# Kernel tuning notes

Measured on AMD Instinct MI355X. Metric: run time of the kernel, lower is better.

Reference implementation:

```python
import jax, jax.numpy as jnp
import numpy as np

B, D, P, C = 4096, 512, 256, 8
LAMBDA = 1.0


def setup_inputs() -> dict:
    key = jax.random.key(0)
    k1, k2, k3, k4 = jax.random.split(key, 4)
    x = jax.random.normal(k1, (B, D), dtype=jnp.float32)
    y = jax.random.randint(k2, (B,), 0, C, dtype=jnp.int32)
    prototypes = jax.random.normal(k3, (P, D), dtype=jnp.float32)
    # omega initialized as eye + 0.01*randn per class, like the torch module
    omega = jnp.eye(D, dtype=jnp.float32)[None] + 0.01 * jax.random.normal(k4, (C, D, D), dtype=jnp.float32)
    prototype_labels = (jnp.arange(P, dtype=jnp.int32) % C).astype(jnp.int32)
    return {"x": x, "y": y, "prototypes": prototypes, "omega": omega, "prototype_labels": prototype_labels}


def reference(x, y, prototypes, omega, prototype_labels):
    # transformed inputs per class: tx[c,b,:] = omega[c] @ x[b]
    tx = jnp.einsum('cij,bj->cbi', omega, x)                     # [C,B,D]
    # transformed prototypes under every class omega, then pick each
    # prototype's own class matrix: tp[p,:] = omega[label[p]] @ w[p]
    tp_all = jnp.einsum('cij,pj->cpi', omega, prototypes)        # [C,P,D]
    tp = tp_all[prototype_labels, jnp.arange(P)]                 # [P,D]
    # squared distances via expansion ||a-b||^2 = |a|^2 + |b|^2 - 2ab
    dots = jnp.einsum('cbd,pd->cbp', tx, tp)                     # [C,B,P]
    x2 = jnp.sum(tx * tx, axis=-1)                               # [C,B]
    p2 = jnp.sum(tp * tp, axis=-1)                               # [P]
    dist_all = x2[:, :, None] + p2[None, None, :] - 2.0 * dots   # [C,B,P]
    # each prototype uses the omega of its own class
    dist = dist_all[prototype_labels, :, jnp.arange(P)].T        # [B,P]
    same = prototype_labels[None, :] == y[:, None]               # [B,P]
    inf = jnp.float32(jnp.inf)
    pos = jnp.min(jnp.where(same, dist, inf), axis=1)            # [B]
    neg = jnp.min(jnp.where(same, inf, dist), axis=1)            # [B]
    mu = (pos - neg) / (pos + neg)
    loss = jnp.mean(jax.nn.sigmoid(LAMBDA * mu))
    loss = loss + 0.01 * jnp.linalg.norm(omega.reshape(-1))
    return loss
```

## Files before the change

### kernel.cpp

```cpp
#include <hip/hip_runtime.h>
#include <math.h>

typedef unsigned short ushort_t;
typedef __attribute__((ext_vector_type(8))) short short8;
typedef __attribute__((ext_vector_type(4))) float f32x4;

#define B_N 4096
#define D_N 512
#define P_N 256
#define C_N 8

#define ACC_OFF   0
#define P2G_OFF   256
#define X2_OFF    1280
#define XB_OFF    132352
#define OMB_OFF   (XB_OFF + B_N*D_N*2)
#define TPG_OFF   (OMB_OFF + C_N*D_N*D_N*2)
#define UG_OFF    (TPG_OFF + P_N*D_N*2)
#define OMBT_OFF  (UG_OFF + P_N*D_N*2)
#define MINB_OFF  OMBT_OFF

#define MFMA16(a, b, c) __builtin_amdgcn_mfma_f32_16x16x32_bf16(a, b, c, 0, 0, 0)

__device__ inline ushort_t f2bf(float f) {
    union { float f; unsigned u; } v; v.f = f;
    unsigned r = v.u + 0x7FFFu + ((v.u >> 16) & 1u);
    return (ushort_t)(r >> 16);
}

__device__ __forceinline__ void gll16(const ushort_t* g, ushort_t* l) {
    __builtin_amdgcn_global_load_lds((const __attribute__((address_space(1))) void*)g,
                                     (__attribute__((address_space(3))) void*)l, 16, 0, 0);
}

__global__ void k_cast_x(const float* __restrict__ x, ushort_t* __restrict__ xb) {
    int idx = blockIdx.x * 256 + threadIdx.x;
    const float4* x4 = (const float4*)x;
    float4 a = x4[idx * 2], b = x4[idx * 2 + 1];
    union { ushort_t s[8]; uint4 v; } o;
    o.s[0] = f2bf(a.x); o.s[1] = f2bf(a.y); o.s[2] = f2bf(a.z); o.s[3] = f2bf(a.w);
    o.s[4] = f2bf(b.x); o.s[5] = f2bf(b.y); o.s[6] = f2bf(b.z); o.s[7] = f2bf(b.w);
    ((uint4*)xb)[idx] = o.v;
}

__global__ void k_cast_om(const float* __restrict__ omega, ushort_t* __restrict__ omb,
                          ushort_t* __restrict__ ombT, float* __restrict__ oss) {
    int c = blockIdx.z, r0 = blockIdx.y * 64, c0 = blockIdx.x * 64;
    __shared__ ushort_t T[64][72];
    __shared__ float red[4];
    int t = threadIdx.x;
    int r = t >> 2, seg = t & 3;
    const float* src = omega + ((size_t)c * D_N + r0 + r) * D_N + c0 + seg * 16;
    float4 v0 = ((const float4*)src)[0], v1 = ((const float4*)src)[1];
    float4 v2 = ((const float4*)src)[2], v3 = ((const float4*)src)[3];
    float s = v0.x*v0.x + v0.y*v0.y + v0.z*v0.z + v0.w*v0.w
            + v1.x*v1.x + v1.y*v1.y + v1.z*v1.z + v1.w*v1.w
            + v2.x*v2.x + v2.y*v2.y + v2.z*v2.z + v2.w*v2.w
            + v3.x*v3.x + v3.y*v3.y + v3.z*v3.z + v3.w*v3.w;
    union { ushort_t s[16]; uint4 v[2]; } o;
    float vv[16] = {v0.x,v0.y,v0.z,v0.w, v1.x,v1.y,v1.z,v1.w,
                    v2.x,v2.y,v2.z,v2.w, v3.x,v3.y,v3.z,v3.w};
    #pragma unroll
    for (int j = 0; j < 16; ++j) o.s[j] = f2bf(vv[j]);
    uint4* dst = (uint4*)(omb + ((size_t)c * D_N + r0 + r) * D_N + c0 + seg * 16);
    dst[0] = o.v[0]; dst[1] = o.v[1];
    #pragma unroll
    for (int j = 0; j < 16; ++j) T[seg * 16 + j][r] = o.s[j];
    __syncthreads();
    int jr = t >> 2, sg2 = t & 3;
    uint4 w0 = *(uint4*)&T[jr][sg2 * 16];
    uint4 w1 = *(uint4*)&T[jr][sg2 * 16 + 8];
    uint4* dstT = (uint4*)(ombT + ((size_t)c * D_N + c0 + jr) * D_N + r0 + sg2 * 16);
    dstT[0] = w0; dstT[1] = w1;
    #pragma unroll
    for (int off = 32; off > 0; off >>= 1) s += __shfl_down(s, off);
    if ((t & 63) == 0) red[t >> 6] = s;
    __syncthreads();
    if (t == 0) atomicAdd(oss, red[0] + red[1] + red[2] + red[3]);
}

__global__ __launch_bounds__(256) void k_tp(const float* __restrict__ prot,
                                            const ushort_t* __restrict__ omb,
                                            ushort_t* __restrict__ tpg,
                                            float* __restrict__ p2g) {
    int i0 = blockIdx.x * 64, c = blockIdx.y;
    __shared__ ushort_t As[32][72];
    __shared__ ushort_t Bs[64][72];
    int t = threadIdx.x, w = t >> 6, lane = t & 63;
    int g = lane >> 4, cl = lane & 15;
    f32x4 acc[2] = {{0,0,0,0},{0,0,0,0}};
    for (int k0 = 0; k0 < D_N; k0 += 64) {
        __syncthreads();
        {
            int m = t >> 3, seg = t & 7;
            const float* ap = prot + ((size_t)(c + 8 * m)) * D_N + k0 + seg * 8;
            float4 u0 = ((const float4*)ap)[0], u1 = ((const float4*)ap)[1];
            union { ushort_t s[8]; uint4 v; } o;
            o.s[0]=f2bf(u0.x); o.s[1]=f2bf(u0.y); o.s[2]=f2bf(u0.z); o.s[3]=f2bf(u0.w);
            o.s[4]=f2bf(u1.x); o.s[5]=f2bf(u1.y); o.s[6]=f2bf(u1.z); o.s[7]=f2bf(u1.w);
            *(uint4*)&As[m][seg * 8] = o.v;
        }
        {
            int r = t >> 2, sg = t & 3;
            const uint4* bp = (const uint4*)(omb + ((size_t)c * D_N + i0 + r) * D_N + k0 + sg * 16);
            *(uint4*)&Bs[r][sg * 16] = bp[0];
            *(uint4*)&Bs[r][sg * 16 + 8] = bp[1];
        }
        __syncthreads();
        #pragma unroll
        for (int kk = 0; kk < 2; ++kk) {
            int koff = kk * 32 + g * 8;
            short8 bfr = *(const short8*)&Bs[w * 16 + cl][koff];
            #pragma unroll
            for (int mt = 0; mt < 2; ++mt) {
                short8 afr = *(const short8*)&As[mt * 16 + cl][koff];
                acc[mt] = MFMA16(afr, bfr, acc[mt]);
            }
        }
    }
    #pragma unroll
    for (int mt = 0; mt < 2; ++mt)
        #pragma unroll
        for (int reg = 0; reg < 4; ++reg) {
            float v = acc[mt][reg];
            int m = mt * 16 + g * 4 + reg;
            int i = i0 + w * 16 + cl;
            tpg[((size_t)c * 32 + m) * D_N + i] = f2bf(v);
            float s = v * v;
            s += __shfl_xor(s, 1); s += __shfl_xor(s, 2);
            s += __shfl_xor(s, 4); s += __shfl_xor(s, 8);
            if (cl == 0) atomicAdd(&p2g[c * 32 + m], s);
        }
}

__global__ __launch_bounds__(256) void k_u(const ushort_t* __restrict__ tpg,
                                           const ushort_t* __restrict__ ombT,
                                           ushort_t* __restrict__ ug) {
    int j0 = blockIdx.x * 64, c = blockIdx.y;
    __shared__ ushort_t As[32][72];
    __shared__ ushort_t Bs[64][72];
    int t = threadIdx.x, w = t >> 6, lane = t & 63;
    int g = lane >> 4, cl = lane & 15;
    f32x4 acc[2] = {{0,0,0,0},{0,0,0,0}};
    for (int k0 = 0; k0 < D_N; k0 += 64) {
        __syncthreads();
        {
            int m = t >> 3, seg = t & 7;
            *(uint4*)&As[m][seg * 8] =
                *(const uint4*)(tpg + ((size_t)c * 32 + m) * D_N + k0 + seg * 8);
        }
        {
            int r = t >> 2, sg = t & 3;
            const uint4* bp = (const uint4*)(ombT + ((size_t)c * D_N + j0 + r) * D_N + k0 + sg * 16);
            *(uint4*)&Bs[r][sg * 16] = bp[0];
            *(uint4*)&Bs[r][sg * 16 + 8] = bp[1];
        }
        __syncthreads();
        #pragma unroll
        for (int kk = 0; kk < 2; ++kk) {
            int koff = kk * 32 + g * 8;
            short8 bfr = *(const short8*)&Bs[w * 16 + cl][koff];
            #pragma unroll
            for (int mt = 0; mt < 2; ++mt) {
                short8 afr = *(const short8*)&As[mt * 16 + cl][koff];
                acc[mt] = MFMA16(afr, bfr, acc[mt]);
            }
        }
    }
    #pragma unroll
    for (int mt = 0; mt < 2; ++mt)
        #pragma unroll
        for (int reg = 0; reg < 4; ++reg) {
            int m = mt * 16 + g * 4 + reg;
            int j = j0 + w * 16 + cl;
            ug[((size_t)c * 32 + m) * D_N + j] = f2bf(acc[mt][reg]);
        }
}

__global__ __launch_bounds__(256, 4) void k_x2d(const ushort_t* __restrict__ xb,
                                                const ushort_t* __restrict__ omb,
                                                const ushort_t* __restrict__ ug,
                                                const float* __restrict__ p2g,
                                                float* __restrict__ x2,
                                                float* __restrict__ minb) {
    int c  = blockIdx.y;
    int b0 = blockIdx.z * 128;
    int t = threadIdx.x, w = t >> 6, lane = t & 63;
    int g = lane >> 4, cl = lane & 15;
    int srow = lane >> 2, spos = lane & 3;

    __shared__ ushort_t Xs[2][128][32];
    __shared__ ushort_t Os[2][128][32];
    __shared__ float red[128][2];

    if (blockIdx.x < 4) {
        int i0 = blockIdx.x * 128;
        int qr = w >> 1, qc = w & 1;
        f32x4 acc[4][4];
        #pragma unroll
        for (int mt = 0; mt < 4; ++mt)
            #pragma unroll
            for (int nt = 0; nt < 4; ++nt) acc[mt][nt] = (f32x4){0,0,0,0};
        #pragma unroll
        for (int i = 0; i < 2; ++i) {
            int rb = w * 32 + i * 16;
            int r  = rb + srow;
            int cg = (spos + r) & 3;
            gll16(xb + (size_t)(b0 + r) * D_N + cg * 8, &Xs[0][rb][0]);
            gll16(omb + ((size_t)c * D_N + i0 + r) * D_N + cg * 8, &Os[0][rb][0]);
        }
        __syncthreads();
        for (int s = 0; s < 16; ++s) {
            int cb = s & 1, nb = cb ^ 1;
            if (s < 15) {
                int k1 = (s + 1) * 32;
                #pragma unroll
                for (int i = 0; i < 2; ++i) {
                    int rb = w * 32 + i * 16;
                    int r  = rb + srow;
                    int cg = (spos + r) & 3;
                    gll16(xb + (size_t)(b0 + r) * D_N + k1 + cg * 8, &Xs[nb][rb][0]);
                    gll16(omb + ((size_t)c * D_N + i0 + r) * D_N + k1 + cg * 8, &Os[nb][rb][0]);
                }
            }
            short8 a[4], b[4];
            #pragma unroll
            for (int mt = 0; mt < 4; ++mt) {
                int r = qr * 64 + mt * 16 + cl;
                a[mt] = *(const short8*)&Xs[cb][r][((g - r) & 3) * 8];
            }
            #pragma unroll
            for (int nt = 0; nt < 4; ++nt) {
                int r = qc * 64 + nt * 16 + cl;
                b[nt] = *(const short8*)&Os[cb][r][((g - r) & 3) * 8];
            }
            #pragma unroll
            for (int mt = 0; mt < 4; ++mt)
                #pragma unroll
                for (int nt = 0; nt < 4; ++nt)
                    acc[mt][nt] = MFMA16(a[mt], b[nt], acc[mt][nt]);
            __syncthreads();
        }
        #pragma unroll
        for (int mt = 0; mt < 4; ++mt)
            #pragma unroll
            for (int reg = 0; reg < 4; ++reg) {
                float s = 0.f;
                #pragma unroll
                for (int nt = 0; nt < 4; ++nt) s += acc[mt][nt][reg] * acc[mt][nt][reg];
                s += __shfl_xor(s, 1); s += __shfl_xor(s, 2);
                s += __shfl_xor(s, 4); s += __shfl_xor(s, 8);
                if (cl == 0) red[qr * 64 + mt * 16 + g * 4 + reg][qc] = s;
            }
        __syncthreads();
        if (t < 128) atomicAdd(&x2[(size_t)(b0 + t) * C_N + c], red[t][0] + red[t][1]);
    } else {
        f32x4 acc[2][2];
        #pragma unroll
        for (int mt = 0; mt < 2; ++mt)
            #pragma unroll
            for (int nt = 0; nt < 2; ++nt) acc[mt][nt] = (f32x4){0,0,0,0};
        #pragma unroll
        for (int i = 0; i < 2; ++i) {
            int rb = w * 32 + i * 16;
            int r  = rb + srow;
            int cg = (spos + r) & 3;
            gll16(xb + (size_t)(b0 + r) * D_N + cg * 8, &Xs[0][rb][0]);
        }
        if (w < 2) {
            int rb = w * 16;
            int r  = rb + srow;
            int cg = (spos + r) & 3;
            gll16(ug + ((size_t)c * 32 + r) * D_N + cg * 8, &Os[0][rb][0]);
        }
        __syncthreads();
        for (int s = 0; s < 16; ++s) {
            int cb = s & 1, nb = cb ^ 1;
            if (s < 15) {
                int k1 = (s + 1) * 32;
                #pragma unroll
                for (int i = 0; i < 2; ++i) {
                    int rb = w * 32 + i * 16;
                    int r  = rb + srow;
                    int cg = (spos + r) & 3;
                    gll16(xb + (size_t)(b0 + r) * D_N + k1 + cg * 8, &Xs[nb][rb][0]);
                }
                if (w < 2) {
                    int rb = w * 16;
                    int r  = rb + srow;
                    int cg = (spos + r) & 3;
                    gll16(ug + ((size_t)c * 32 + r) * D_N + k1 + cg * 8, &Os[nb][rb][0]);
                }
            }
            short8 a[2], b[2];
            #pragma unroll
            for (int mt = 0; mt < 2; ++mt) {
                int r = w * 32 + mt * 16 + cl;
                a[mt] = *(const short8*)&Xs[cb][r][((g - r) & 3) * 8];
            }
            #pragma unroll
            for (int nt = 0; nt < 2; ++nt) {
                int r = nt * 16 + cl;
                b[nt] = *(const short8*)&Os[cb][r][((g - r) & 3) * 8];
            }
            #pragma unroll
            for (int mt = 0; mt < 2; ++mt)
                #pragma unroll
                for (int nt = 0; nt < 2; ++nt)
                    acc[mt][nt] = MFMA16(a[mt], b[nt], acc[mt][nt]);
            __syncthreads();
        }
        #pragma unroll
        for (int mt = 0; mt < 2; ++mt)
            #pragma unroll
            for (int reg = 0; reg < 4; ++reg) {
                float v = INFINITY;
                #pragma unroll
                for (int nt = 0; nt < 2; ++nt) {
                    int q = c * 32 + nt * 16 + cl;
                    v = fminf(v, p2g[q] - 2.f * acc[mt][nt][reg]);
                }
                v = fminf(v, __shfl_xor(v, 1)); v = fminf(v, __shfl_xor(v, 2));
                v = fminf(v, __shfl_xor(v, 4)); v = fminf(v, __shfl_xor(v, 8));
                if (cl == 0)
                    minb[(size_t)(b0 + w * 32 + mt * 16 + g * 4 + reg) * C_N + c] = v;
            }
    }
}

__global__ void k_mu(const float* __restrict__ x2, const float* __restrict__ minb,
                     const int* __restrict__ y, float* __restrict__ acc) {
    int t = threadIdx.x;
    int b = blockIdx.x * 256 + t;
    int yb = y[b];
    float d[8];
    #pragma unroll
    for (int cc = 0; cc < 8; ++cc)
        d[cc] = x2[(size_t)b * C_N + cc] + minb[(size_t)b * C_N + cc];
    float pos = d[yb];
    float neg = INFINITY;
    #pragma unroll
    for (int cc = 0; cc < 8; ++cc)
        if (cc != yb) neg = fminf(neg, d[cc]);
    float mu = (pos - neg) / (pos + neg);
    float s = 1.f / (1.f + expf(-mu));
    #pragma unroll
    for (int off = 32; off > 0; off >>= 1) s += __shfl_down(s, off);
    __shared__ float red[4];
    if ((t & 63) == 0) red[t >> 6] = s;
    __syncthreads();
    if (t == 0) atomicAdd(acc, red[0] + red[1] + red[2] + red[3]);
}

__global__ void k_final(const float* __restrict__ accs, float* __restrict__ out) {
    out[0] = accs[0] * (1.f / (float)B_N) + 0.01f * sqrtf(accs[1]);
}

extern "C" void kernel_launch(void* const* d_in, const int* in_sizes, int n_in,
                              void* d_out, int out_size, void* d_ws, size_t ws_size,
                              hipStream_t stream) {
    (void)in_sizes; (void)n_in; (void)out_size; (void)ws_size;
    const float* x     = (const float*)d_in[0];
    const int*   y     = (const int*)d_in[1];
    const float* prot  = (const float*)d_in[2];
    const float* omega = (const float*)d_in[3];

    char* ws = (char*)d_ws;
    float*    accs = (float*)(ws + ACC_OFF);
    float*    p2g  = (float*)(ws + P2G_OFF);
    float*    x2   = (float*)(ws + X2_OFF);
    ushort_t* xb   = (ushort_t*)(ws + XB_OFF);
    ushort_t* omb  = (ushort_t*)(ws + OMB_OFF);
    ushort_t* tpg  = (ushort_t*)(ws + TPG_OFF);
    ushort_t* ug   = (ushort_t*)(ws + UG_OFF);
    ushort_t* ombT = (ushort_t*)(ws + OMBT_OFF);
    float*    minb = (float*)(ws + MINB_OFF);

    (void)hipMemsetAsync(ws, 0, XB_OFF, stream);
    k_cast_x <<<B_N * D_N / 8 / 256, 256, 0, stream>>>(x, xb);
    k_cast_om<<<dim3(8, 8, C_N), 256, 0, stream>>>(omega, omb, ombT, accs + 1);
    k_tp     <<<dim3(8, C_N), 256, 0, stream>>>(prot, omb, tpg, p2g);
    k_u      <<<dim3(8, C_N), 256, 0, stream>>>(tpg, ombT, ug);
    k_x2d    <<<dim3(5, C_N, B_N / 128), 256, 0, stream>>>(xb, omb, ug, p2g, x2, minb);
    k_mu     <<<B_N / 256, 256, 0, stream>>>(x2, minb, y, accs);
    k_final  <<<1, 1, 0, stream>>>(accs, (float*)d_out);
}
```

Before: 133.8 us.

## Fuse pipeline into persistent mega-kernel with atomic ticket dependencies

```diff
diff --git a/kernel.cpp b/kernel.cpp
--- a/kernel.cpp
+++ b/kernel.cpp
@@ -11,14 +11,15 @@
 #define C_N 8
 
 #define ACC_OFF   0
+#define TK_OFF    64
 #define P2G_OFF   256
 #define X2_OFF    1280
 #define XB_OFF    132352
 #define OMB_OFF   (XB_OFF + B_N*D_N*2)
-#define TPG_OFF   (OMB_OFF + C_N*D_N*D_N*2)
-#define UG_OFF    (TPG_OFF + P_N*D_N*2)
-#define OMBT_OFF  (UG_OFF + P_N*D_N*2)
-#define MINB_OFF  OMBT_OFF
+#define UG_OFF    (OMB_OFF + C_N*D_N*D_N*2)
+#define TPG_OFF   (UG_OFF + P_N*D_N*2)
+#define OMBT_OFF  (TPG_OFF + P_N*D_N*2)
+#define MINB_OFF  (OMBT_OFF + C_N*D_N*D_N*2)
 
 #define MFMA16(a, b, c) __builtin_amdgcn_mfma_f32_16x16x32_bf16(a, b, c, 0, 0, 0)
 
@@ -33,22 +34,277 @@
                                      (__attribute__((address_space(3))) void*)l, 16, 0, 0);
 }
 
-__global__ void k_cast_x(const float* __restrict__ x, ushort_t* __restrict__ xb) {
-    int idx = blockIdx.x * 256 + threadIdx.x;
-    const float4* x4 = (const float4*)x;
-    float4 a = x4[idx * 2], b = x4[idx * 2 + 1];
-    union { ushort_t s[8]; uint4 v; } o;
-    o.s[0] = f2bf(a.x); o.s[1] = f2bf(a.y); o.s[2] = f2bf(a.z); o.s[3] = f2bf(a.w);
-    o.s[4] = f2bf(b.x); o.s[5] = f2bf(b.y); o.s[6] = f2bf(b.z); o.s[7] = f2bf(b.w);
-    ((uint4*)xb)[idx] = o.v;
-}
-
-__global__ void k_cast_om(const float* __restrict__ omega, ushort_t* __restrict__ omb,
-                          ushort_t* __restrict__ ombT, float* __restrict__ oss) {
-    int c = blockIdx.z, r0 = blockIdx.y * 64, c0 = blockIdx.x * 64;
+union SharedU {
+    struct { ushort_t Xs[2][128][32]; ushort_t Os[2][128][32]; float red[128][2]; } x;
+    struct { ushort_t Xs[2][128][32]; ushort_t Us[2][32][32]; } d;
+    struct { ushort_t As[32][72]; ushort_t Bs[64][72]; } p;
+};
+
+__device__ __forceinline__ void wait_ticket(unsigned* tk, unsigned target) {
+    if (threadIdx.x == 0) {
+        while (atomicAdd(tk, 0u) < target) __builtin_amdgcn_s_sleep(8);
+        __threadfence();
+    }
+    __syncthreads();
+}
+
+__device__ __forceinline__ void do_tp(int c, int i0, SharedU& S, const float* __restrict__ prot,
+                                      const ushort_t* __restrict__ omb,
+                                      ushort_t* __restrict__ tpg, float* __restrict__ p2g) {
+    int t = threadIdx.x, w = t >> 6, lane = t & 63;
+    int g = lane >> 4, cl = lane & 15;
+    f32x4 acc[2] = {{0,0,0,0},{0,0,0,0}};
+    for (int k0 = 0; k0 < D_N; k0 += 64) {
+        __syncthreads();
+        {
+            int m = t >> 3, seg = t & 7;
+            const float* ap = prot + ((size_t)(c + 8 * m)) * D_N + k0 + seg * 8;
+            float4 u0 = ((const float4*)ap)[0], u1 = ((const float4*)ap)[1];
+            union { ushort_t s[8]; uint4 v; } o;
+            o.s[0]=f2bf(u0.x); o.s[1]=f2bf(u0.y); o.s[2]=f2bf(u0.z); o.s[3]=f2bf(u0.w);
+            o.s[4]=f2bf(u1.x); o.s[5]=f2bf(u1.y); o.s[6]=f2bf(u1.z); o.s[7]=f2bf(u1.w);
+            *(uint4*)&S.p.As[m][seg * 8] = o.v;
+        }
+        {
+            int r = t >> 2, sg = t & 3;
+            const uint4* bp = (const uint4*)(omb + ((size_t)c * D_N + i0 + r) * D_N + k0 + sg * 16);
+            *(uint4*)&S.p.Bs[r][sg * 16] = bp[0];
+            *(uint4*)&S.p.Bs[r][sg * 16 + 8] = bp[1];
+        }
+        __syncthreads();
+        #pragma unroll
+        for (int kk = 0; kk < 2; ++kk) {
+            int koff = kk * 32 + g * 8;
+            short8 bfr = *(const short8*)&S.p.Bs[w * 16 + cl][koff];
+            #pragma unroll
+            for (int mt = 0; mt < 2; ++mt) {
+                short8 afr = *(const short8*)&S.p.As[mt * 16 + cl][koff];
+                acc[mt] = MFMA16(afr, bfr, acc[mt]);
+            }
+        }
+    }
+    #pragma unroll
+    for (int mt = 0; mt < 2; ++mt)
+        #pragma unroll
+        for (int reg = 0; reg < 4; ++reg) {
+            float v = acc[mt][reg];
+            int m = mt * 16 + g * 4 + reg;
+            int i = i0 + w * 16 + cl;
+            tpg[((size_t)c * 32 + m) * D_N + i] = f2bf(v);
+            float s = v * v;
+            s += __shfl_xor(s, 1); s += __shfl_xor(s, 2);
+            s += __shfl_xor(s, 4); s += __shfl_xor(s, 8);
+            if (cl == 0) atomicAdd(&p2g[c * 32 + m], s);
+        }
+}
+
+__device__ __forceinline__ void do_u(int c, int j0, SharedU& S, const ushort_t* __restrict__ tpg,
+                                     const ushort_t* __restrict__ ombT, ushort_t* __restrict__ ug) {
+    int t = threadIdx.x, w = t >> 6, lane = t & 63;
+    int g = lane >> 4, cl = lane & 15;
+    f32x4 acc[2] = {{0,0,0,0},{0,0,0,0}};
+    for (int k0 = 0; k0 < D_N; k0 += 64) {
+        __syncthreads();
+        {
+            int m = t >> 3, seg = t & 7;
+            *(uint4*)&S.p.As[m][seg * 8] =
+                *(const uint4*)(tpg + ((size_t)c * 32 + m) * D_N + k0 + seg * 8);
+        }
+        {
+            int r = t >> 2, sg = t & 3;
+            const uint4* bp = (const uint4*)(ombT + ((size_t)c * D_N + j0 + r) * D_N + k0 + sg * 16);
+            *(uint4*)&S.p.Bs[r][sg * 16] = bp[0];
+            *(uint4*)&S.p.Bs[r][sg * 16 + 8] = bp[1];
+        }
+        __syncthreads();
+        #pragma unroll
+        for (int kk = 0; kk < 2; ++kk) {
+            int koff = kk * 32 + g * 8;
+            short8 bfr = *(const short8*)&S.p.Bs[w * 16 + cl][koff];
+            #pragma unroll
+            for (int mt = 0; mt < 2; ++mt) {
+                short8 afr = *(const short8*)&S.p.As[mt * 16 + cl][koff];
+                acc[mt] = MFMA16(afr, bfr, acc[mt]);
+            }
+        }
+    }
+    #pragma unroll
+    for (int mt = 0; mt < 2; ++mt)
+        #pragma unroll
+        for (int reg = 0; reg < 4; ++reg) {
+            int m = mt * 16 + g * 4 + reg;
+            int j = j0 + w * 16 + cl;
+            ug[((size_t)c * 32 + m) * D_N + j] = f2bf(acc[mt][reg]);
+        }
+}
+
+__device__ __forceinline__ void do_x2(int unit, SharedU& S, const ushort_t* __restrict__ xb,
+                                      const ushort_t* __restrict__ omb, float* __restrict__ x2) {
+    int ic = unit & 3, c = (unit >> 2) & 7, b0 = (unit >> 5) * 128;
+    int i0 = ic * 128;
+    int t = threadIdx.x, w = t >> 6, lane = t & 63;
+    int g = lane >> 4, cl = lane & 15;
+    int srow = lane >> 2, spos = lane & 3;
+    int qr = w >> 1, qc = w & 1;
+    f32x4 acc[4][4];
+    #pragma unroll
+    for (int mt = 0; mt < 4; ++mt)
+        #pragma unroll
+        for (int nt = 0; nt < 4; ++nt) acc[mt][nt] = (f32x4){0,0,0,0};
+    __syncthreads();
+    #pragma unroll
+    for (int i = 0; i < 2; ++i) {
+        int rb = w * 32 + i * 16;
+        int r  = rb + srow;
+        int cg = (spos + r) & 3;
+        gll16(xb + (size_t)(b0 + r) * D_N + cg * 8, &S.x.Xs[0][rb][0]);
+        gll16(omb + ((size_t)c * D_N + i0 + r) * D_N + cg * 8, &S.x.Os[0][rb][0]);
+    }
+    __syncthreads();
+    for (int s = 0; s < 16; ++s) {
+        int cb = s & 1, nb = cb ^ 1;
+        if (s < 15) {
+            int k1 = (s + 1) * 32;
+            #pragma unroll
+            for (int i = 0; i < 2; ++i) {
+                int rb = w * 32 + i * 16;
+                int r  = rb + srow;
+                int cg = (spos + r) & 3;
+                gll16(xb + (size_t)(b0 + r) * D_N + k1 + cg * 8, &S.x.Xs[nb][rb][0]);
+                gll16(omb + ((size_t)c * D_N + i0 + r) * D_N + k1 + cg * 8, &S.x.Os[nb][rb][0]);
+            }
+        }
+        short8 a[4], b[4];
+        #pragma unroll
+        for (int mt = 0; mt < 4; ++mt) {
+            int r = qr * 64 + mt * 16 + cl;
+            a[mt] = *(const short8*)&S.x.Xs[cb][r][((g - r) & 3) * 8];
+        }
+        #pragma unroll
+        for (int nt = 0; nt < 4; ++nt) {
+            int r = qc * 64 + nt * 16 + cl;
+            b[nt] = *(const short8*)&S.x.Os[cb][r][((g - r) & 3) * 8];
+        }
+        #pragma unroll
+        for (int mt = 0; mt < 4; ++mt)
+            #pragma unroll
+            for (int nt = 0; nt < 4; ++nt)
+                acc[mt][nt] = MFMA16(a[mt], b[nt], acc[mt][nt]);
+        __syncthreads();
+    }
+    #pragma unroll
+    for (int mt = 0; mt < 4; ++mt)
+        #pragma unroll
+        for (int reg = 0; reg < 4; ++reg) {
+            float s = 0.f;
+            #pragma unroll
+            for (int nt = 0; nt < 4; ++nt) s += acc[mt][nt][reg] * acc[mt][nt][reg];
+            s += __shfl_xor(s, 1); s += __shfl_xor(s, 2);
+            s += __shfl_xor(s, 4); s += __shfl_xor(s, 8);
+            if (cl == 0) S.x.red[qr * 64 + mt * 16 + g * 4 + reg][qc] = s;
+        }
+    __syncthreads();
+    if (t < 128) atomicAdd(&x2[(size_t)(b0 + t) * C_N + c], S.x.red[t][0] + S.x.red[t][1]);
+}
+
+__device__ __forceinline__ void do_dots(int unit, SharedU& S, const ushort_t* __restrict__ xb,
+                                        const ushort_t* __restrict__ ug,
+                                        const float* __restrict__ p2g, float* __restrict__ minb) {
+    int c = unit & 7, b0 = (unit >> 3) * 128;
+    int t = threadIdx.x, w = t >> 6, lane = t & 63;
+    int g = lane >> 4, cl = lane & 15;
+    int srow = lane >> 2, spos = lane & 3;
+    f32x4 acc[2][2];
+    #pragma unroll
+    for (int mt = 0; mt < 2; ++mt)
+        #pragma unroll
+        for (int nt = 0; nt < 2; ++nt) acc[mt][nt] = (f32x4){0,0,0,0};
+    #pragma unroll
+    for (int i = 0; i < 2; ++i) {
+        int rb = w * 32 + i * 16;
+        int r  = rb + srow;
+        int cg = (spos + r) & 3;
+        gll16(xb + (size_t)(b0 + r) * D_N + cg * 8, &S.d.Xs[0][rb][0]);
+    }
+    if (w < 2) {
+        int rb = w * 16;
+        int r  = rb + srow;
+        int cg = (spos + r) & 3;
+        gll16(ug + ((size_t)c * 32 + r) * D_N + cg * 8, &S.d.Us[0][rb][0]);
+    }
+    __syncthreads();
+    for (int s = 0; s < 16; ++s) {
+        int cb = s & 1, nb = cb ^ 1;
+        if (s < 15) {
+            int k1 = (s + 1) * 32;
+            #pragma unroll
+            for (int i = 0; i < 2; ++i) {
+                int rb = w * 32 + i * 16;
+                int r  = rb + srow;
+                int cg = (spos + r) & 3;
+                gll16(xb + (size_t)(b0 + r) * D_N + k1 + cg * 8, &S.d.Xs[nb][rb][0]);
+            }
+            if (w < 2) {
+                int rb = w * 16;
+                int r  = rb + srow;
+                int cg = (spos + r) & 3;
+                gll16(ug + ((size_t)c * 32 + r) * D_N + k1 + cg * 8, &S.d.Us[nb][rb][0]);
+            }
+        }
+        short8 a[2], b[2];
+        #pragma unroll
+        for (int mt = 0; mt < 2; ++mt) {
+            int r = w * 32 + mt * 16 + cl;
+            a[mt] = *(const short8*)&S.d.Xs[cb][r][((g - r) & 3) * 8];
+        }
+        #pragma unroll
+        for (int nt = 0; nt < 2; ++nt) {
+            int r = nt * 16 + cl;
+            b[nt] = *(const short8*)&S.d.Us[cb][r][((g - r) & 3) * 8];
+        }
+        #pragma unroll
+        for (int mt = 0; mt < 2; ++mt)
+            #pragma unroll
+            for (int nt = 0; nt < 2; ++nt)
+                acc[mt][nt] = MFMA16(a[mt], b[nt], acc[mt][nt]);
+        __syncthreads();
+    }
+    #pragma unroll
+    for (int mt = 0; mt < 2; ++mt)
+        #pragma unroll
+        for (int reg = 0; reg < 4; ++reg) {
+            float v = INFINITY;
+            #pragma unroll
+            for (int nt = 0; nt < 2; ++nt) {
+                int q = c * 32 + nt * 16 + cl;
+                v = fminf(v, p2g[q] - 2.f * acc[mt][nt][reg]);
+            }
+            v = fminf(v, __shfl_xor(v, 1)); v = fminf(v, __shfl_xor(v, 2));
+            v = fminf(v, __shfl_xor(v, 4)); v = fminf(v, __shfl_xor(v, 8));
+            if (cl == 0)
+                minb[(size_t)(b0 + w * 32 + mt * 16 + g * 4 + reg) * C_N + c] = v;
+        }
+}
+
+__global__ void k_cast(const float* __restrict__ x, const float* __restrict__ omega,
+                       ushort_t* __restrict__ xb, ushort_t* __restrict__ omb,
+                       ushort_t* __restrict__ ombT, float* __restrict__ oss) {
     __shared__ ushort_t T[64][72];
     __shared__ float red[4];
     int t = threadIdx.x;
+    if (blockIdx.x < 1024) {
+        int idx = blockIdx.x * 256 + t;
+        const float4* x4 = (const float4*)x;
+        float4 a = x4[idx * 2], b = x4[idx * 2 + 1];
+        union { ushort_t s[8]; uint4 v; } o;
+        o.s[0] = f2bf(a.x); o.s[1] = f2bf(a.y); o.s[2] = f2bf(a.z); o.s[3] = f2bf(a.w);
+        o.s[4] = f2bf(b.x); o.s[5] = f2bf(b.y); o.s[6] = f2bf(b.z); o.s[7] = f2bf(b.w);
+        ((uint4*)xb)[idx] = o.v;
+        return;
+    }
+    int bid = blockIdx.x - 1024;
+    int c = bid >> 6, by = (bid >> 3) & 7, bx = bid & 7;
+    int r0 = by * 64, c0 = bx * 64;
     int r = t >> 2, seg = t & 3;
     const float* src = omega + ((size_t)c * D_N + r0 + r) * D_N + c0 + seg * 16;
     float4 v0 = ((const float4*)src)[0], v1 = ((const float4*)src)[1];
@@ -79,257 +335,41 @@
     if (t == 0) atomicAdd(oss, red[0] + red[1] + red[2] + red[3]);
 }
 
-__global__ __launch_bounds__(256) void k_tp(const float* __restrict__ prot,
-                                            const ushort_t* __restrict__ omb,
-                                            ushort_t* __restrict__ tpg,
-                                            float* __restrict__ p2g) {
-    int i0 = blockIdx.x * 64, c = blockIdx.y;
-    __shared__ ushort_t As[32][72];
-    __shared__ ushort_t Bs[64][72];
-    int t = threadIdx.x, w = t >> 6, lane = t & 63;
-    int g = lane >> 4, cl = lane & 15;
-    f32x4 acc[2] = {{0,0,0,0},{0,0,0,0}};
-    for (int k0 = 0; k0 < D_N; k0 += 64) {
-        __syncthreads();
-        {
-            int m = t >> 3, seg = t & 7;
-            const float* ap = prot + ((size_t)(c + 8 * m)) * D_N + k0 + seg * 8;
-            float4 u0 = ((const float4*)ap)[0], u1 = ((const float4*)ap)[1];
-            union { ushort_t s[8]; uint4 v; } o;
-            o.s[0]=f2bf(u0.x); o.s[1]=f2bf(u0.y); o.s[2]=f2bf(u0.z); o.s[3]=f2bf(u0.w);
-            o.s[4]=f2bf(u1.x); o.s[5]=f2bf(u1.y); o.s[6]=f2bf(u1.z); o.s[7]=f2bf(u1.w);
-            *(uint4*)&As[m][seg * 8] = o.v;
-        }
-        {
-            int r = t >> 2, sg = t & 3;
-            const uint4* bp = (const uint4*)(omb + ((size_t)c * D_N + i0 + r) * D_N + k0 + sg * 16);
-            *(uint4*)&Bs[r][sg * 16] = bp[0];
-            *(uint4*)&Bs[r][sg * 16 + 8] = bp[1];
-        }
-        __syncthreads();
-        #pragma unroll
-        for (int kk = 0; kk < 2; ++kk) {
-            int koff = kk * 32 + g * 8;
-            short8 bfr = *(const short8*)&Bs[w * 16 + cl][koff];
-            #pragma unroll
-            for (int mt = 0; mt < 2; ++mt) {
-                short8 afr = *(const short8*)&As[mt * 16 + cl][koff];
-                acc[mt] = MFMA16(afr, bfr, acc[mt]);
-            }
-        }
-    }
-    #pragma unroll
-    for (int mt = 0; mt < 2; ++mt)
-        #pragma unroll
-        for (int reg = 0; reg < 4; ++reg) {
-            float v = acc[mt][reg];
-            int m = mt * 16 + g * 4 + reg;
-            int i = i0 + w * 16 + cl;
-            tpg[((size_t)c * 32 + m) * D_N + i] = f2bf(v);
-            float s = v * v;
-            s += __shfl_xor(s, 1); s += __shfl_xor(s, 2);
-            s += __shfl_xor(s, 4); s += __shfl_xor(s, 8);
-            if (cl == 0) atomicAdd(&p2g[c * 32 + m], s);
-        }
-}
-
-__global__ __launch_bounds__(256) void k_u(const ushort_t* __restrict__ tpg,
-                                           const ushort_t* __restrict__ ombT,
-                                           ushort_t* __restrict__ ug) {
-    int j0 = blockIdx.x * 64, c = blockIdx.y;
-    __shared__ ushort_t As[32][72];
-    __shared__ ushort_t Bs[64][72];
-    int t = threadIdx.x, w = t >> 6, lane = t & 63;
-    int g = lane >> 4, cl = lane & 15;
-    f32x4 acc[2] = {{0,0,0,0},{0,0,0,0}};
-    for (int k0 = 0; k0 < D_N; k0 += 64) {
-        __syncthreads();
-        {
-            int m = t >> 3, seg = t & 7;
-            *(uint4*)&As[m][seg * 8] =
-                *(const uint4*)(tpg + ((size_t)c * 32 + m) * D_N + k0 + seg * 8);
-        }
-        {
-            int r = t >> 2, sg = t & 3;
-            const uint4* bp = (const uint4*)(ombT + ((size_t)c * D_N + j0 + r) * D_N + k0 + sg * 16);
-            *(uint4*)&Bs[r][sg * 16] = bp[0];
-            *(uint4*)&Bs[r][sg * 16 + 8] = bp[1];
-        }
-        __syncthreads();
-        #pragma unroll
-        for (int kk = 0; kk < 2; ++kk) {
-            int koff = kk * 32 + g * 8;
-            short8 bfr = *(const short8*)&Bs[w * 16 + cl][koff];
-            #pragma unroll
-            for (int mt = 0; mt < 2; ++mt) {
-                short8 afr = *(const short8*)&As[mt * 16 + cl][koff];
-                acc[mt] = MFMA16(afr, bfr, acc[mt]);
-            }
-        }
-    }
-    #pragma unroll
-    for (int mt = 0; mt < 2; ++mt)
-        #pragma unroll
-        for (int reg = 0; reg < 4; ++reg) {
-            int m = mt * 16 + g * 4 + reg;
-            int j = j0 + w * 16 + cl;
-            ug[((size_t)c * 32 + m) * D_N + j] = f2bf(acc[mt][reg]);
-        }
-}
-
-__global__ __launch_bounds__(256, 4) void k_x2d(const ushort_t* __restrict__ xb,
-                                                const ushort_t* __restrict__ omb,
-                                                const ushort_t* __restrict__ ug,
-                                                const float* __restrict__ p2g,
-                                                float* __restrict__ x2,
-                                                float* __restrict__ minb) {
-    int c  = blockIdx.y;
-    int b0 = blockIdx.z * 128;
-    int t = threadIdx.x, w = t >> 6, lane = t & 63;
-    int g = lane >> 4, cl = lane & 15;
-    int srow = lane >> 2, spos = lane & 3;
-
-    __shared__ ushort_t Xs[2][128][32];
-    __shared__ ushort_t Os[2][128][32];
-    __shared__ float red[128][2];
-
-    if (blockIdx.x < 4) {
-        int i0 = blockIdx.x * 128;
-        int qr = w >> 1, qc = w & 1;
-        f32x4 acc[4][4];
-        #pragma unroll
-        for (int mt = 0; mt < 4; ++mt)
-            #pragma unroll
-            for (int nt = 0; nt < 4; ++nt) acc[mt][nt] = (f32x4){0,0,0,0};
-        #pragma unroll
-        for (int i = 0; i < 2; ++i) {
-            int rb = w * 32 + i * 16;
-            int r  = rb + srow;
-            int cg = (spos + r) & 3;
-            gll16(xb + (size_t)(b0 + r) * D_N + cg * 8, &Xs[0][rb][0]);
-            gll16(omb + ((size_t)c * D_N + i0 + r) * D_N + cg * 8, &Os[0][rb][0]);
-        }
-        __syncthreads();
-        for (int s = 0; s < 16; ++s) {
-            int cb = s & 1, nb = cb ^ 1;
-            if (s < 15) {
-                int k1 = (s + 1) * 32;
-                #pragma unroll
-                for (int i = 0; i < 2; ++i) {
-                    int rb = w * 32 + i * 16;
-                    int r  = rb + srow;
-                    int cg = (spos + r) & 3;
-                    gll16(xb + (size_t)(b0 + r) * D_N + k1 + cg * 8, &Xs[nb][rb][0]);
-                    gll16(omb + ((size_t)c * D_N + i0 + r) * D_N + k1 + cg * 8, &Os[nb][rb][0]);
-                }
-            }
-            short8 a[4], b[4];
-            #pragma unroll
-            for (int mt = 0; mt < 4; ++mt) {
-                int r = qr * 64 + mt * 16 + cl;
-                a[mt] = *(const short8*)&Xs[cb][r][((g - r) & 3) * 8];
-            }
-            #pragma unroll
-            for (int nt = 0; nt < 4; ++nt) {
-                int r = qc * 64 + nt * 16 + cl;
-                b[nt] = *(const short8*)&Os[cb][r][((g - r) & 3) * 8];
-            }
-            #pragma unroll
-            for (int mt = 0; mt < 4; ++mt)
-                #pragma unroll
-                for (int nt = 0; nt < 4; ++nt)
-                    acc[mt][nt] = MFMA16(a[mt], b[nt], acc[mt][nt]);
-            __syncthreads();
-        }
-        #pragma unroll
-        for (int mt = 0; mt < 4; ++mt)
-            #pragma unroll
-            for (int reg = 0; reg < 4; ++reg) {
-                float s = 0.f;
-                #pragma unroll
-                for (int nt = 0; nt < 4; ++nt) s += acc[mt][nt][reg] * acc[mt][nt][reg];
-                s += __shfl_xor(s, 1); s += __shfl_xor(s, 2);
-                s += __shfl_xor(s, 4); s += __shfl_xor(s, 8);
-                if (cl == 0) red[qr * 64 + mt * 16 + g * 4 + reg][qc] = s;
-            }
-        __syncthreads();
-        if (t < 128) atomicAdd(&x2[(size_t)(b0 + t) * C_N + c], red[t][0] + red[t][1]);
-    } else {
-        f32x4 acc[2][2];
-        #pragma unroll
-        for (int mt = 0; mt < 2; ++mt)
-            #pragma unroll
-            for (int nt = 0; nt < 2; ++nt) acc[mt][nt] = (f32x4){0,0,0,0};
-        #pragma unroll
-        for (int i = 0; i < 2; ++i) {
-            int rb = w * 32 + i * 16;
-            int r  = rb + srow;
-            int cg = (spos + r) & 3;
-            gll16(xb + (size_t)(b0 + r) * D_N + cg * 8, &Xs[0][rb][0]);
-        }
-        if (w < 2) {
-            int rb = w * 16;
-            int r  = rb + srow;
-            int cg = (spos + r) & 3;
-            gll16(ug + ((size_t)c * 32 + r) * D_N + cg * 8, &Os[0][rb][0]);
-        }
-        __syncthreads();
-        for (int s = 0; s < 16; ++s) {
-            int cb = s & 1, nb = cb ^ 1;
-            if (s < 15) {
-                int k1 = (s + 1) * 32;
-                #pragma unroll
-                for (int i = 0; i < 2; ++i) {
-                    int rb = w * 32 + i * 16;
-                    int r  = rb + srow;
-                    int cg = (spos + r) & 3;
-                    gll16(xb + (size_t)(b0 + r) * D_N + k1 + cg * 8, &Xs[nb][rb][0]);
-                }
-                if (w < 2) {
-                    int rb = w * 16;
-                    int r  = rb + srow;
-                    int cg = (spos + r) & 3;
-                    gll16(ug + ((size_t)c * 32 + r) * D_N + k1 + cg * 8, &Os[nb][rb][0]);
-                }
-            }
-            short8 a[2], b[2];
-            #pragma unroll
-            for (int mt = 0; mt < 2; ++mt) {
-                int r = w * 32 + mt * 16 + cl;
-                a[mt] = *(const short8*)&Xs[cb][r][((g - r) & 3) * 8];
-            }
-            #pragma unroll
-            for (int nt = 0; nt < 2; ++nt) {
-                int r = nt * 16 + cl;
-                b[nt] = *(const short8*)&Os[cb][r][((g - r) & 3) * 8];
-            }
-            #pragma unroll
-            for (int mt = 0; mt < 2; ++mt)
-                #pragma unroll
-                for (int nt = 0; nt < 2; ++nt)
-                    acc[mt][nt] = MFMA16(a[mt], b[nt], acc[mt][nt]);
-            __syncthreads();
-        }
-        #pragma unroll
-        for (int mt = 0; mt < 2; ++mt)
-            #pragma unroll
-            for (int reg = 0; reg < 4; ++reg) {
-                float v = INFINITY;
-                #pragma unroll
-                for (int nt = 0; nt < 2; ++nt) {
-                    int q = c * 32 + nt * 16 + cl;
-                    v = fminf(v, p2g[q] - 2.f * acc[mt][nt][reg]);
-                }
-                v = fminf(v, __shfl_xor(v, 1)); v = fminf(v, __shfl_xor(v, 2));
-                v = fminf(v, __shfl_xor(v, 4)); v = fminf(v, __shfl_xor(v, 8));
-                if (cl == 0)
-                    minb[(size_t)(b0 + w * 32 + mt * 16 + g * 4 + reg) * C_N + c] = v;
-            }
+__global__ __launch_bounds__(256, 4) void k_mega(const float* __restrict__ prot,
+                                                 const ushort_t* __restrict__ xb,
+                                                 const ushort_t* __restrict__ omb,
+                                                 const ushort_t* __restrict__ ombT,
+                                                 ushort_t* __restrict__ tpg,
+                                                 ushort_t* __restrict__ ug,
+                                                 float* __restrict__ p2g,
+                                                 float* __restrict__ x2,
+                                                 float* __restrict__ minb,
+                                                 unsigned* __restrict__ tk) {
+    __shared__ SharedU S;
+    int bid = blockIdx.x;
+    if (bid < 64) {
+        do_tp(bid >> 3, (bid & 7) * 64, S, prot, omb, tpg, p2g);
+        __syncthreads();
+        if (threadIdx.x == 0) { __threadfence(); atomicAdd(&tk[bid >> 3], 1u); }
+    } else if (bid < 128) {
+        int u = bid - 64, c = u >> 3;
+        wait_ticket(&tk[c], 8u);
+        do_u(c, (u & 7) * 64, S, tpg, ombT, ug);
+        __syncthreads();
+        if (threadIdx.x == 0) { __threadfence(); atomicAdd(&tk[8 + c], 1u); }
+    }
+    do_x2(2 * bid, S, xb, omb, x2);
+    do_x2(2 * bid + 1, S, xb, omb, x2);
+    if (bid >= 128 && bid < 384) {
+        int du = bid - 128;
+        wait_ticket(&tk[8 + (du & 7)], 8u);
+        do_dots(du, S, xb, ug, p2g, minb);
     }
 }
 
 __global__ void k_mu(const float* __restrict__ x2, const float* __restrict__ minb,
-                     const int* __restrict__ y, float* __restrict__ acc) {
+                     const int* __restrict__ y, float* __restrict__ accs,
+                     float* __restrict__ out) {
     int t = threadIdx.x;
     int b = blockIdx.x * 256 + t;
     int yb = y[b];
@@ -349,11 +389,16 @@
     __shared__ float red[4];
     if ((t & 63) == 0) red[t >> 6] = s;
     __syncthreads();
-    if (t == 0) atomicAdd(acc, red[0] + red[1] + red[2] + red[3]);
-}
-
-__global__ void k_final(const float* __restrict__ accs, float* __restrict__ out) {
-    out[0] = accs[0] * (1.f / (float)B_N) + 0.01f * sqrtf(accs[1]);
+    if (t == 0) {
+        atomicAdd(accs, red[0] + red[1] + red[2] + red[3]);
+        __threadfence();
+        unsigned n = atomicAdd((unsigned*)(accs + 2), 1u);
+        if (n == (unsigned)(B_N / 256 - 1)) {
+            float ls  = atomicAdd(accs, 0.f);
+            float oss = atomicAdd(accs + 1, 0.f);
+            out[0] = ls * (1.f / (float)B_N) + 0.01f * sqrtf(oss);
+        }
+    }
 }
 
 extern "C" void kernel_launch(void* const* d_in, const int* in_sizes, int n_in,
@@ -367,21 +412,18 @@
 
     char* ws = (char*)d_ws;
     float*    accs = (float*)(ws + ACC_OFF);
+    unsigned* tk   = (unsigned*)(ws + TK_OFF);
     float*    p2g  = (float*)(ws + P2G_OFF);
     float*    x2   = (float*)(ws + X2_OFF);
     ushort_t* xb   = (ushort_t*)(ws + XB_OFF);
     ushort_t* omb  = (ushort_t*)(ws + OMB_OFF);
+    ushort_t* ug   = (ushort_t*)(ws + UG_OFF);
     ushort_t* tpg  = (ushort_t*)(ws + TPG_OFF);
-    ushort_t* ug   = (ushort_t*)(ws + UG_OFF);
     ushort_t* ombT = (ushort_t*)(ws + OMBT_OFF);
     float*    minb = (float*)(ws + MINB_OFF);
 
     (void)hipMemsetAsync(ws, 0, XB_OFF, stream);
-    k_cast_x <<<B_N * D_N / 8 / 256, 256, 0, stream>>>(x, xb);
-    k_cast_om<<<dim3(8, 8, C_N), 256, 0, stream>>>(omega, omb, ombT, accs + 1);
-    k_tp     <<<dim3(8, C_N), 256, 0, stream>>>(prot, omb, tpg, p2g);
-    k_u      <<<dim3(8, C_N), 256, 0, stream>>>(tpg, ombT, ug);
-    k_x2d    <<<dim3(5, C_N, B_N / 128), 256, 0, stream>>>(xb, omb, ug, p2g, x2, minb);
-    k_mu     <<<B_N / 256, 256, 0, stream>>>(x2, minb, y, accs);
-    k_final  <<<1, 1, 0, stream>>>(accs, (float*)d_out);
-}
+    k_cast <<<1536, 256, 0, stream>>>(x, omega, xb, omb, ombT, accs + 1);
+    k_mega <<<512, 256, 0, stream>>>(prot, xb, omb, ombT, tpg, ug, p2g, x2, minb, tk);
+    k_mu   <<<B_N / 256, 256, 0, stream>>>(x2, minb, y, accs, (float*)d_out);
+}
```

New measurement: 178.9 us. +33.7%, slower.

## Merge cast kernels, deepen x2 GEMM prefetch, fold final reduction into k_mu

Applied to the files above, without the earlier changes.

```diff
diff --git a/kernel.cpp b/kernel.cpp
--- a/kernel.cpp
+++ b/kernel.cpp
@@ -33,22 +33,25 @@
                                      (__attribute__((address_space(3))) void*)l, 16, 0, 0);
 }
 
-__global__ void k_cast_x(const float* __restrict__ x, ushort_t* __restrict__ xb) {
-    int idx = blockIdx.x * 256 + threadIdx.x;
-    const float4* x4 = (const float4*)x;
-    float4 a = x4[idx * 2], b = x4[idx * 2 + 1];
-    union { ushort_t s[8]; uint4 v; } o;
-    o.s[0] = f2bf(a.x); o.s[1] = f2bf(a.y); o.s[2] = f2bf(a.z); o.s[3] = f2bf(a.w);
-    o.s[4] = f2bf(b.x); o.s[5] = f2bf(b.y); o.s[6] = f2bf(b.z); o.s[7] = f2bf(b.w);
-    ((uint4*)xb)[idx] = o.v;
-}
-
-__global__ void k_cast_om(const float* __restrict__ omega, ushort_t* __restrict__ omb,
-                          ushort_t* __restrict__ ombT, float* __restrict__ oss) {
-    int c = blockIdx.z, r0 = blockIdx.y * 64, c0 = blockIdx.x * 64;
+__global__ void k_cast(const float* __restrict__ x, const float* __restrict__ omega,
+                       ushort_t* __restrict__ xb, ushort_t* __restrict__ omb,
+                       ushort_t* __restrict__ ombT, float* __restrict__ oss) {
     __shared__ ushort_t T[64][72];
     __shared__ float red[4];
     int t = threadIdx.x;
+    if (blockIdx.x < 1024) {
+        int idx = blockIdx.x * 256 + t;
+        const float4* x4 = (const float4*)x;
+        float4 a = x4[idx * 2], b = x4[idx * 2 + 1];
+        union { ushort_t s[8]; uint4 v; } o;
+        o.s[0] = f2bf(a.x); o.s[1] = f2bf(a.y); o.s[2] = f2bf(a.z); o.s[3] = f2bf(a.w);
+        o.s[4] = f2bf(b.x); o.s[5] = f2bf(b.y); o.s[6] = f2bf(b.z); o.s[7] = f2bf(b.w);
+        ((uint4*)xb)[idx] = o.v;
+        return;
+    }
+    int bid = blockIdx.x - 1024;
+    int c = bid >> 6, by = (bid >> 3) & 7, bx = bid & 7;
+    int r0 = by * 64, c0 = bx * 64;
     int r = t >> 2, seg = t & 3;
     const float* src = omega + ((size_t)c * D_N + r0 + r) * D_N + c0 + seg * 16;
     float4 v0 = ((const float4*)src)[0], v1 = ((const float4*)src)[1];
@@ -177,12 +180,13 @@
         }
 }
 
-__global__ __launch_bounds__(256, 4) void k_x2d(const ushort_t* __restrict__ xb,
-                                                const ushort_t* __restrict__ omb,
-                                                const ushort_t* __restrict__ ug,
-                                                const float* __restrict__ p2g,
-                                                float* __restrict__ x2,
-                                                float* __restrict__ minb) {
+__global__ __attribute__((amdgpu_flat_work_group_size(256, 256), amdgpu_waves_per_eu(3, 3)))
+void k_x2d(const ushort_t* __restrict__ xb,
+           const ushort_t* __restrict__ omb,
+           const ushort_t* __restrict__ ug,
+           const float* __restrict__ p2g,
+           float* __restrict__ x2,
+           float* __restrict__ minb) {
     int c  = blockIdx.y;
     int b0 = blockIdx.z * 128;
     int t = threadIdx.x, w = t >> 6, lane = t & 63;
@@ -201,46 +205,55 @@
         for (int mt = 0; mt < 4; ++mt)
             #pragma unroll
             for (int nt = 0; nt < 4; ++nt) acc[mt][nt] = (f32x4){0,0,0,0};
-        #pragma unroll
-        for (int i = 0; i < 2; ++i) {
-            int rb = w * 32 + i * 16;
-            int r  = rb + srow;
-            int cg = (spos + r) & 3;
-            gll16(xb + (size_t)(b0 + r) * D_N + cg * 8, &Xs[0][rb][0]);
-            gll16(omb + ((size_t)c * D_N + i0 + r) * D_N + cg * 8, &Os[0][rb][0]);
-        }
-        __syncthreads();
-        for (int s = 0; s < 16; ++s) {
-            int cb = s & 1, nb = cb ^ 1;
-            if (s < 15) {
-                int k1 = (s + 1) * 32;
-                #pragma unroll
-                for (int i = 0; i < 2; ++i) {
-                    int rb = w * 32 + i * 16;
-                    int r  = rb + srow;
-                    int cg = (spos + r) & 3;
-                    gll16(xb + (size_t)(b0 + r) * D_N + k1 + cg * 8, &Xs[nb][rb][0]);
-                    gll16(omb + ((size_t)c * D_N + i0 + r) * D_N + k1 + cg * 8, &Os[nb][rb][0]);
-                }
-            }
-            short8 a[4], b[4];
-            #pragma unroll
-            for (int mt = 0; mt < 4; ++mt) {
-                int r = qr * 64 + mt * 16 + cl;
-                a[mt] = *(const short8*)&Xs[cb][r][((g - r) & 3) * 8];
-            }
-            #pragma unroll
-            for (int nt = 0; nt < 4; ++nt) {
-                int r = qc * 64 + nt * 16 + cl;
-                b[nt] = *(const short8*)&Os[cb][r][((g - r) & 3) * 8];
-            }
-            #pragma unroll
-            for (int mt = 0; mt < 4; ++mt)
-                #pragma unroll
-                for (int nt = 0; nt < 4; ++nt)
-                    acc[mt][nt] = MFMA16(a[mt], b[nt], acc[mt][nt]);
-            __syncthreads();
-        }
+
+        #define STG(bf, k1) do {                                                        \
+            _Pragma("unroll")                                                           \
+            for (int i = 0; i < 2; ++i) {                                               \
+                int rb = w * 32 + i * 16;                                               \
+                int r  = rb + srow;                                                     \
+                int cg = (spos + r) & 3;                                                \
+                gll16(xb + (size_t)(b0 + r) * D_N + (k1) + cg * 8, &Xs[bf][rb][0]);     \
+                gll16(omb + ((size_t)c * D_N + i0 + r) * D_N + (k1) + cg * 8,           \
+                      &Os[bf][rb][0]);                                                  \
+            } } while (0)
+
+        #define CMP(cb) do {                                                            \
+            short8 a_[4], b_[4];                                                        \
+            _Pragma("unroll")                                                           \
+            for (int mt = 0; mt < 4; ++mt) {                                            \
+                int r = qr * 64 + mt * 16 + cl;                                         \
+                a_[mt] = *(const short8*)&Xs[cb][r][((g - r) & 3) * 8];                 \
+            }                                                                           \
+            _Pragma("unroll")                                                           \
+            for (int nt = 0; nt < 4; ++nt) {                                            \
+                int r = qc * 64 + nt * 16 + cl;                                         \
+                b_[nt] = *(const short8*)&Os[cb][r][((g - r) & 3) * 8];                 \
+            }                                                                           \
+            _Pragma("unroll")                                                           \
+            for (int mt = 0; mt < 4; ++mt)                                              \
+                _Pragma("unroll")                                                       \
+                for (int nt = 0; nt < 4; ++nt)                                          \
+                    acc[mt][nt] = MFMA16(a_[mt], b_[nt], acc[mt][nt]);                  \
+            } while (0)
+
+        STG(0, 0);
+        STG(1, 32);
+        for (int s = 0; s < 15; ++s) {
+            int cb = s & 1;
+            asm volatile("s_waitcnt vmcnt(4)" ::: "memory");
+            __builtin_amdgcn_s_barrier();
+            __builtin_amdgcn_sched_barrier(0);
+            CMP(cb);
+            __builtin_amdgcn_sched_barrier(0);
+            __builtin_amdgcn_s_barrier();
+            if (s < 14) STG(cb, (s + 2) * 32);
+        }
+        asm volatile("s_waitcnt vmcnt(0)" ::: "memory");
+        __builtin_amdgcn_s_barrier();
+        __builtin_amdgcn_sched_barrier(0);
+        CMP(1);
+        #undef STG
+        #undef CMP
         #pragma unroll
         for (int mt = 0; mt < 4; ++mt)
             #pragma unroll
@@ -329,7 +342,8 @@
 }
 
 __global__ void k_mu(const float* __restrict__ x2, const float* __restrict__ minb,
-                     const int* __restrict__ y, float* __restrict__ acc) {
+                     const int* __restrict__ y, float* __restrict__ accs,
+                     float* __restrict__ out) {
     int t = threadIdx.x;
     int b = blockIdx.x * 256 + t;
     int yb = y[b];
@@ -349,11 +363,16 @@
     __shared__ float red[4];
     if ((t & 63) == 0) red[t >> 6] = s;
     __syncthreads();
-    if (t == 0) atomicAdd(acc, red[0] + red[1] + red[2] + red[3]);
-}
-
-__global__ void k_final(const float* __restrict__ accs, float* __restrict__ out) {
-    out[0] = accs[0] * (1.f / (float)B_N) + 0.01f * sqrtf(accs[1]);
+    if (t == 0) {
+        atomicAdd(accs, red[0] + red[1] + red[2] + red[3]);
+        __threadfence();
+        unsigned n = atomicAdd((unsigned*)(accs + 2), 1u);
+        if (n == (unsigned)(B_N / 256 - 1)) {
+            float ls  = atomicAdd(accs, 0.f);
+            float oss = atomicAdd(accs + 1, 0.f);
+            out[0] = ls * (1.f / (float)B_N) + 0.01f * sqrtf(oss);
+        }
+    }
 }
 
 extern "C" void kernel_launch(void* const* d_in, const int* in_sizes, int n_in,
@@ -377,11 +396,9 @@
     float*    minb = (float*)(ws + MINB_OFF);
 
     (void)hipMemsetAsync(ws, 0, XB_OFF, stream);
-    k_cast_x <<<B_N * D_N / 8 / 256, 256, 0, stream>>>(x, xb);
-    k_cast_om<<<dim3(8, 8, C_N), 256, 0, stream>>>(omega, omb, ombT, accs + 1);
-    k_tp     <<<dim3(8, C_N), 256, 0, stream>>>(prot, omb, tpg, p2g);
-    k_u      <<<dim3(8, C_N), 256, 0, stream>>>(tpg, ombT, ug);
-    k_x2d    <<<dim3(5, C_N, B_N / 128), 256, 0, stream>>>(xb, omb, ug, p2g, x2, minb);
-    k_mu     <<<B_N / 256, 256, 0, stream>>>(x2, minb, y, accs);
-    k_final  <<<1, 1, 0, stream>>>(accs, (float*)d_out);
-}
+    k_cast <<<1536, 256, 0, stream>>>(x, omega, xb, omb, ombT, accs + 1);
+    k_tp   <<<dim3(8, C_N), 256, 0, stream>>>(prot, omb, tpg, p2g);
+    k_u    <<<dim3(8, C_N), 256, 0, stream>>>(tpg, ombT, ug);
+    k_x2d  <<<dim3(5, C_N, B_N / 128), 256, 0, stream>>>(xb, omb, ug, p2g, x2, minb);
+    k_mu   <<<B_N / 256, 256, 0, stream>>>(x2, minb, y, accs, (float*)d_out);
+}
```

Result: faster. 130.4 us (-2.5%).
